# Optimization experiments

Hardware: AMD Instinct MI355X
Metric: run time of the kernel (lower is better)

Reference implementation:

```python
import jax, jax.numpy as jnp
import numpy as np

N = 8192        # nodes
NFEAT = 256     # input feature dim
NHID = 64       # per-head hidden dim
NHEADS = 4
NCLASS = 121    # PPI label count
ALPHA = 0.2     # LeakyReLU negative slope
NEG_INF = jnp.float32(-9e15)  # pyGAT's mask fill value


def setup_inputs() -> dict:
    key = jax.random.key(0)
    k = jax.random.split(key, 6)
    x = jax.random.normal(k[0], (N, NFEAT), dtype=jnp.float32)
    adj = (jax.random.uniform(k[1], (N, N)) < 0.01).astype(jnp.float32)
    idx = jnp.arange(N)
    adj = adj.at[idx, idx].set(1.0)
    # per-head first-layer params: W [H, nfeat, nhid], a [H, 2*nhid]
    Ws = jax.random.normal(k[2], (NHEADS, NFEAT, NHID), dtype=jnp.float32) * 0.1
    a_heads = jax.random.normal(k[3], (NHEADS, 2 * NHID), dtype=jnp.float32) * 0.1
    # output attention layer params
    W_out = jax.random.normal(k[4], (NHEADS * NHID, NCLASS), dtype=jnp.float32) * 0.1
    a_out = jax.random.normal(k[5], (2 * NCLASS,), dtype=jnp.float32) * 0.1
    return {"x": x, "adj": adj, "Ws": Ws, "a_heads": a_heads,
            "W_out": W_out, "a_out": a_out}


def _gat_head(x, adj, W, a, concat):
    # Dense GraphAttentionLayer (pyGAT), eval mode (dropout off).
    Wh = x @ W                                   # [N, d]
    d = W.shape[1]
    f_src = Wh @ a[:d]                           # [N]  score contribution of node i
    f_dst = Wh @ a[d:]                           # [N]  score contribution of node j
    e = jax.nn.leaky_relu(f_src[:, None] + f_dst[None, :], ALPHA)  # [N, N]
    e = jnp.where(adj > 0, e, NEG_INF)
    att = jax.nn.softmax(e, axis=-1)             # [N, N]
    h = att @ Wh                                 # [N, d]
    return jax.nn.elu(h) if concat else h


def reference(x, adj, Ws, a_heads, W_out, a_out):
    # first multi-head layer (concat=True, elu), vmapped over heads
    heads = jax.vmap(lambda W, a: _gat_head(x, adj, W, a, True))(Ws, a_heads)  # [H, N, nhid]
    h_cat = jnp.transpose(heads, (1, 0, 2)).reshape(x.shape[0], NHEADS * NHID)  # torch.cat(dim=1)
    # output attention layer (concat=False -> raw aggregation)
    return _gat_head(h_cat, adj, W_out, a_out, False)  # [N, nclass]
```

## Files before the change

kernel.cpp:

```cpp
#include <hip/hip_runtime.h>
#include <math.h>

#define N_NODES 8192
#define NFEAT 256
#define NHID 64
#define NHEADS 4
#define NCLASS 121
#define NCPAD 128
#define CAP 256
#define LRALPHA 0.2f

__global__ __launch_bounds__(256) void build_csr(const float* __restrict__ adj,
                                                 int* __restrict__ nbr,
                                                 int* __restrict__ deg) {
    int row = blockIdx.x;
    __shared__ int cnt;
    if (threadIdx.x == 0) cnt = 0;
    __syncthreads();
    const float4* arow = (const float4*)(adj + (size_t)row * N_NODES);
    for (int j4 = threadIdx.x; j4 < N_NODES / 4; j4 += 256) {
        float4 v = arow[j4];
        if (v.x > 0.f) { int s = atomicAdd(&cnt, 1); if (s < CAP) nbr[row * CAP + s] = j4 * 4 + 0; }
        if (v.y > 0.f) { int s = atomicAdd(&cnt, 1); if (s < CAP) nbr[row * CAP + s] = j4 * 4 + 1; }
        if (v.z > 0.f) { int s = atomicAdd(&cnt, 1); if (s < CAP) nbr[row * CAP + s] = j4 * 4 + 2; }
        if (v.w > 0.f) { int s = atomicAdd(&cnt, 1); if (s < CAP) nbr[row * CAP + s] = j4 * 4 + 3; }
    }
    __syncthreads();
    if (threadIdx.x == 0) deg[row] = cnt < CAP ? cnt : CAP;
}

__global__ __launch_bounds__(256) void pad_params(const float* __restrict__ Wout,
                                                  const float* __restrict__ aout,
                                                  float* __restrict__ Wpad,
                                                  float* __restrict__ apad) {
    int idx = blockIdx.x * 256 + threadIdx.x;
    if (idx < 256 * NCPAD) {
        int k = idx >> 7, c = idx & 127;
        Wpad[idx] = (c < NCLASS) ? Wout[k * NCLASS + c] : 0.f;
    }
    if (idx < 256) {
        int c = idx & 127;
        float v = 0.f;
        if (c < NCLASS) v = (idx < 128) ? aout[c] : aout[NCLASS + c];
        apad[idx] = v;
    }
}

__global__ __launch_bounds__(256) void gemm1(const float* __restrict__ x,
                                             const float* __restrict__ Ws,
                                             float* __restrict__ Wh1) {
    int h = blockIdx.y;
    int r0 = blockIdx.x * 64;
    __shared__ float xs[64][260];
    for (int t = threadIdx.x; t < 64 * 64; t += 256) {
        int r = t >> 6, c4 = t & 63;
        *(float4*)&xs[r][c4 * 4] = *(const float4*)(x + (size_t)(r0 + r) * NFEAT + c4 * 4);
    }
    __syncthreads();
    int d = threadIdx.x & 63;
    int rb = (threadIdx.x >> 6) * 16;
    const float* W = Ws + (size_t)h * NFEAT * NHID + d;
    float acc[16] = {};
    for (int k4 = 0; k4 < NFEAT; k4 += 4) {
        float b0 = W[(k4 + 0) * NHID];
        float b1 = W[(k4 + 1) * NHID];
        float b2 = W[(k4 + 2) * NHID];
        float b3 = W[(k4 + 3) * NHID];
#pragma unroll
        for (int r = 0; r < 16; r++) {
            float4 a = *(const float4*)&xs[rb + r][k4];
            acc[r] += a.x * b0 + a.y * b1 + a.z * b2 + a.w * b3;
        }
    }
#pragma unroll
    for (int r = 0; r < 16; r++)
        Wh1[((size_t)(r0 + rb + r) * NHEADS + h) * NHID + d] = acc[r];
}

__global__ __launch_bounds__(256) void attn_coef1(const float* __restrict__ Wh1,
                                                  const float* __restrict__ a_heads,
                                                  float* __restrict__ fs1,
                                                  float* __restrict__ fd1) {
    int i = blockIdx.x;
    int h = threadIdx.x >> 6, lane = threadIdx.x & 63;
    float wh = Wh1[((size_t)i * NHEADS + h) * NHID + lane];
    float s = wh * a_heads[h * 2 * NHID + lane];
    float dd = wh * a_heads[h * 2 * NHID + NHID + lane];
#pragma unroll
    for (int o = 32; o > 0; o >>= 1) { s += __shfl_down(s, o); dd += __shfl_down(dd, o); }
    if (lane == 0) { fs1[h * N_NODES + i] = s; fd1[h * N_NODES + i] = dd; }
}

__global__ __launch_bounds__(256) void attn_agg1(const int* __restrict__ nbr,
                                                 const int* __restrict__ deg,
                                                 const float* __restrict__ Wh1,
                                                 const float* __restrict__ fs1,
                                                 const float* __restrict__ fd1,
                                                 float* __restrict__ hcat) {
    int i = blockIdx.x;
    int h = threadIdx.x >> 6, lane = threadIdx.x & 63;
    __shared__ float ebuf[NHEADS][CAP + 1];
    __shared__ int nbrs[CAP];
    __shared__ float inv_s[NHEADS];
    __shared__ float part[NHEADS][256];
    int dg = deg[i];
    for (int t = threadIdx.x; t < dg; t += 256) nbrs[t] = nbr[i * CAP + t];
    __syncthreads();
    float fsi = fs1[h * N_NODES + i];
    const float* fdh = fd1 + h * N_NODES;
    float m = -3.4e38f;
    for (int t = lane; t < dg; t += 64) {
        float e = fsi + fdh[nbrs[t]];
        e = e > 0.f ? e : LRALPHA * e;
        ebuf[h][t] = e;
        m = fmaxf(m, e);
    }
#pragma unroll
    for (int o = 32; o > 0; o >>= 1) m = fmaxf(m, __shfl_xor(m, o));
    float s = 0.f;
    for (int t = lane; t < dg; t += 64) {
        float p = __expf(ebuf[h][t] - m);
        ebuf[h][t] = p;
        s += p;
    }
#pragma unroll
    for (int o = 32; o > 0; o >>= 1) s += __shfl_xor(s, o);
    if (lane == 0) inv_s[h] = 1.f / s;
    __syncthreads();
    int w = h;
    int hh = lane >> 4;
    float4 acc = make_float4(0.f, 0.f, 0.f, 0.f);
    int t = w;
    for (; t + 8 <= dg; t += 8) {
        int j0 = nbrs[t], j1 = nbrs[t + 4];
        float4 v0 = ((const float4*)(Wh1 + (size_t)j0 * 256))[lane];
        float4 v1 = ((const float4*)(Wh1 + (size_t)j1 * 256))[lane];
        float p0 = ebuf[hh][t], p1 = ebuf[hh][t + 4];
        acc.x += p0 * v0.x; acc.y += p0 * v0.y; acc.z += p0 * v0.z; acc.w += p0 * v0.w;
        acc.x += p1 * v1.x; acc.y += p1 * v1.y; acc.z += p1 * v1.z; acc.w += p1 * v1.w;
    }
    for (; t < dg; t += 4) {
        int j = nbrs[t];
        float4 v = ((const float4*)(Wh1 + (size_t)j * 256))[lane];
        float p = ebuf[hh][t];
        acc.x += p * v.x; acc.y += p * v.y; acc.z += p * v.z; acc.w += p * v.w;
    }
    ((float4*)part[w])[lane] = acc;
    __syncthreads();
    int dim = threadIdx.x;
    float r = part[0][dim] + part[1][dim] + part[2][dim] + part[3][dim];
    r *= inv_s[dim >> 6];
    r = r > 0.f ? r : expm1f(r);
    hcat[(size_t)i * 256 + dim] = r;
}

__global__ __launch_bounds__(256) void gemm2(const float* __restrict__ hcat,
                                             const float* __restrict__ Wpad,
                                             float* __restrict__ Wh2) {
    int r0 = blockIdx.x * 64;
    __shared__ float xs[64][260];
    for (int t = threadIdx.x; t < 64 * 64; t += 256) {
        int r = t >> 6, c4 = t & 63;
        *(float4*)&xs[r][c4 * 4] = *(const float4*)(hcat + (size_t)(r0 + r) * 256 + c4 * 4);
    }
    __syncthreads();
    int c0 = (threadIdx.x & 63) * 2;
    int rb = (threadIdx.x >> 6) * 16;
    float acc0[16] = {}, acc1[16] = {};
    for (int k4 = 0; k4 < 256; k4 += 4) {
        float2 b0 = *(const float2*)&Wpad[(k4 + 0) * NCPAD + c0];
        float2 b1 = *(const float2*)&Wpad[(k4 + 1) * NCPAD + c0];
        float2 b2 = *(const float2*)&Wpad[(k4 + 2) * NCPAD + c0];
        float2 b3 = *(const float2*)&Wpad[(k4 + 3) * NCPAD + c0];
#pragma unroll
        for (int r = 0; r < 16; r++) {
            float4 a = *(const float4*)&xs[rb + r][k4];
            acc0[r] += a.x * b0.x + a.y * b1.x + a.z * b2.x + a.w * b3.x;
            acc1[r] += a.x * b0.y + a.y * b1.y + a.z * b2.y + a.w * b3.y;
        }
    }
#pragma unroll
    for (int r = 0; r < 16; r++) {
        float2 v = make_float2(acc0[r], acc1[r]);
        *(float2*)&Wh2[(size_t)(r0 + rb + r) * NCPAD + c0] = v;
    }
}

__global__ __launch_bounds__(256) void attn_coef2(const float* __restrict__ Wh2,
                                                  const float* __restrict__ apad,
                                                  float* __restrict__ fs2,
                                                  float* __restrict__ fd2) {
    int i = blockIdx.x * 4 + (threadIdx.x >> 6);
    int lane = threadIdx.x & 63;
    float w0 = Wh2[(size_t)i * NCPAD + lane];
    float w1 = Wh2[(size_t)i * NCPAD + 64 + lane];
    float s = w0 * apad[lane] + w1 * apad[64 + lane];
    float dd = w0 * apad[128 + lane] + w1 * apad[192 + lane];
#pragma unroll
    for (int o = 32; o > 0; o >>= 1) { s += __shfl_down(s, o); dd += __shfl_down(dd, o); }
    if (lane == 0) { fs2[i] = s; fd2[i] = dd; }
}

__global__ __launch_bounds__(256) void attn_agg2(const int* __restrict__ nbr,
                                                 const int* __restrict__ deg,
                                                 const float* __restrict__ Wh2,
                                                 const float* __restrict__ fs2,
                                                 const float* __restrict__ fd2,
                                                 float* __restrict__ out) {
    int i = blockIdx.x;
    int w = threadIdx.x >> 6, lane = threadIdx.x & 63;
    __shared__ float ebuf[CAP];
    __shared__ int nbrs[CAP];
    __shared__ float red[4];
    __shared__ float part[4][128];
    __shared__ float inv_s;
    int dg = deg[i];
    for (int t = threadIdx.x; t < dg; t += 256) nbrs[t] = nbr[i * CAP + t];
    __syncthreads();
    float fsi = fs2[i];
    float m = -3.4e38f;
    for (int t = threadIdx.x; t < dg; t += 256) {
        float e = fsi + fd2[nbrs[t]];
        e = e > 0.f ? e : LRALPHA * e;
        ebuf[t] = e;
        m = fmaxf(m, e);
    }
#pragma unroll
    for (int o = 32; o > 0; o >>= 1) m = fmaxf(m, __shfl_xor(m, o));
    if (lane == 0) red[w] = m;
    __syncthreads();
    m = fmaxf(fmaxf(red[0], red[1]), fmaxf(red[2], red[3]));
    float s = 0.f;
    for (int t = threadIdx.x; t < dg; t += 256) {
        float p = __expf(ebuf[t] - m);
        ebuf[t] = p;
        s += p;
    }
#pragma unroll
    for (int o = 32; o > 0; o >>= 1) s += __shfl_xor(s, o);
    __syncthreads();
    if (lane == 0) red[w] = s;
    __syncthreads();
    if (threadIdx.x == 0) inv_s = 1.f / (red[0] + red[1] + red[2] + red[3]);
    __syncthreads();
    float2 acc = make_float2(0.f, 0.f);
    int t = w;
    for (; t + 8 <= dg; t += 8) {
        int j0 = nbrs[t], j1 = nbrs[t + 4];
        float2 v0 = ((const float2*)(Wh2 + (size_t)j0 * NCPAD))[lane];
        float2 v1 = ((const float2*)(Wh2 + (size_t)j1 * NCPAD))[lane];
        float p0 = ebuf[t], p1 = ebuf[t + 4];
        acc.x += p0 * v0.x; acc.y += p0 * v0.y;
        acc.x += p1 * v1.x; acc.y += p1 * v1.y;
    }
    for (; t < dg; t += 4) {
        int j = nbrs[t];
        float2 v = ((const float2*)(Wh2 + (size_t)j * NCPAD))[lane];
        float p = ebuf[t];
        acc.x += p * v.x; acc.y += p * v.y;
    }
    ((float2*)part[w])[lane] = acc;
    __syncthreads();
    if (threadIdx.x < NCPAD) {
        int dim = threadIdx.x;
        float r = (part[0][dim] + part[1][dim] + part[2][dim] + part[3][dim]) * inv_s;
        if (dim < NCLASS) out[(size_t)i * NCLASS + dim] = r;
    }
}


extern "C" void kernel_launch(void* const* d_in, const int* in_sizes, int n_in,
                              void* d_out, int out_size, void* d_ws, size_t ws_size,
                              hipStream_t stream) {
    const float* x       = (const float*)d_in[0];
    const float* adj     = (const float*)d_in[1];
    const float* Ws      = (const float*)d_in[2];
    const float* a_heads = (const float*)d_in[3];
    const float* Wout    = (const float*)d_in[4];
    const float* aout    = (const float*)d_in[5];
    float* out = (float*)d_out;

    char* ws = (char*)d_ws;
    size_t off = 0;
    auto alloc = [&](size_t bytes) { void* p = ws + off; off = (off + bytes + 255) & ~(size_t)255; return p; };
    int*   nbr  = (int*)  alloc((size_t)N_NODES * CAP * 4);
    int*   deg  = (int*)  alloc((size_t)N_NODES * 4);
    float* Wh1  = (float*)alloc((size_t)N_NODES * NHEADS * NHID * 4);
    float* fs1  = (float*)alloc((size_t)NHEADS * N_NODES * 4);
    float* fd1  = (float*)alloc((size_t)NHEADS * N_NODES * 4);
    float* hcat = (float*)alloc((size_t)N_NODES * NHEADS * NHID * 4);
    float* Wh2  = (float*)alloc((size_t)N_NODES * NCPAD * 4);
    float* fs2  = (float*)alloc((size_t)N_NODES * 4);
    float* fd2  = (float*)alloc((size_t)N_NODES * 4);
    float* Wpad = (float*)alloc((size_t)256 * NCPAD * 4);
    float* apad = (float*)alloc((size_t)256 * 4);

    build_csr<<<N_NODES, 256, 0, stream>>>(adj, nbr, deg);
    pad_params<<<128, 256, 0, stream>>>(Wout, aout, Wpad, apad);
    gemm1<<<dim3(N_NODES / 64, NHEADS), 256, 0, stream>>>(x, Ws, Wh1);
    attn_coef1<<<N_NODES, 256, 0, stream>>>(Wh1, a_heads, fs1, fd1);
    attn_agg1<<<N_NODES, 256, 0, stream>>>(nbr, deg, Wh1, fs1, fd1, hcat);
    gemm2<<<N_NODES / 64, 256, 0, stream>>>(hcat, Wpad, Wh2);
    attn_coef2<<<N_NODES / 4, 256, 0, stream>>>(Wh2, apad, fs2, fd2);
    attn_agg2<<<N_NODES, 256, 0, stream>>>(nbr, deg, Wh2, fs2, fd2, out);
}
```

Measured before the change: 532.8 us.

## Fuse CSR build, param padding, layer-1 GEMM and attention coefficients into one launch

Merges build_csr, pad_params and gemm1 into a single heterogeneous kernel that dispatches on block index. The GEMM blocks now compute all four heads at once and reduce the attention source/destination scores in-register. The layer-2 coefficient computation is folded into gemm2's epilogue the same way. This removes four kernel launches and the re-reads of Wh1/Wh2 by the separate coefficient kernels. In exchange, the GEMM blocks carry much higher register pressure (64 accumulators plus 16 weight values per thread), and only 128 GEMM blocks share the grid with the 8192 CSR blocks.

```diff
diff --git a/kernel.cpp b/kernel.cpp
--- a/kernel.cpp
+++ b/kernel.cpp
@@ -10,85 +10,120 @@
 #define CAP 256
 #define LRALPHA 0.2f
 
-__global__ __launch_bounds__(256) void build_csr(const float* __restrict__ adj,
-                                                 int* __restrict__ nbr,
-                                                 int* __restrict__ deg) {
-    int row = blockIdx.x;
-    __shared__ int cnt;
-    if (threadIdx.x == 0) cnt = 0;
-    __syncthreads();
-    const float4* arow = (const float4*)(adj + (size_t)row * N_NODES);
-    for (int j4 = threadIdx.x; j4 < N_NODES / 4; j4 += 256) {
-        float4 v = arow[j4];
-        if (v.x > 0.f) { int s = atomicAdd(&cnt, 1); if (s < CAP) nbr[row * CAP + s] = j4 * 4 + 0; }
-        if (v.y > 0.f) { int s = atomicAdd(&cnt, 1); if (s < CAP) nbr[row * CAP + s] = j4 * 4 + 1; }
-        if (v.z > 0.f) { int s = atomicAdd(&cnt, 1); if (s < CAP) nbr[row * CAP + s] = j4 * 4 + 2; }
-        if (v.w > 0.f) { int s = atomicAdd(&cnt, 1); if (s < CAP) nbr[row * CAP + s] = j4 * 4 + 3; }
-    }
-    __syncthreads();
-    if (threadIdx.x == 0) deg[row] = cnt < CAP ? cnt : CAP;
-}
-
-__global__ __launch_bounds__(256) void pad_params(const float* __restrict__ Wout,
-                                                  const float* __restrict__ aout,
-                                                  float* __restrict__ Wpad,
-                                                  float* __restrict__ apad) {
-    int idx = blockIdx.x * 256 + threadIdx.x;
-    if (idx < 256 * NCPAD) {
-        int k = idx >> 7, c = idx & 127;
-        Wpad[idx] = (c < NCLASS) ? Wout[k * NCLASS + c] : 0.f;
-    }
-    if (idx < 256) {
-        int c = idx & 127;
-        float v = 0.f;
-        if (c < NCLASS) v = (idx < 128) ? aout[c] : aout[NCLASS + c];
-        apad[idx] = v;
-    }
-}
-
-__global__ __launch_bounds__(256) void gemm1(const float* __restrict__ x,
-                                             const float* __restrict__ Ws,
-                                             float* __restrict__ Wh1) {
-    int h = blockIdx.y;
-    int r0 = blockIdx.x * 64;
-    __shared__ float xs[64][260];
-    for (int t = threadIdx.x; t < 64 * 64; t += 256) {
-        int r = t >> 6, c4 = t & 63;
-        *(float4*)&xs[r][c4 * 4] = *(const float4*)(x + (size_t)(r0 + r) * NFEAT + c4 * 4);
-    }
-    __syncthreads();
-    int d = threadIdx.x & 63;
-    int rb = (threadIdx.x >> 6) * 16;
-    const float* W = Ws + (size_t)h * NFEAT * NHID + d;
-    float acc[16] = {};
-    for (int k4 = 0; k4 < NFEAT; k4 += 4) {
-        float b0 = W[(k4 + 0) * NHID];
-        float b1 = W[(k4 + 1) * NHID];
-        float b2 = W[(k4 + 2) * NHID];
-        float b3 = W[(k4 + 3) * NHID];
+#define GEMM_BLOCKS 128
+#define CSR_BASE    GEMM_BLOCKS
+#define PAD_BLOCK   (CSR_BASE + N_NODES)
+
+__global__ __launch_bounds__(256) void fused_A(const float* __restrict__ adj,
+                                               const float* __restrict__ x,
+                                               const float* __restrict__ Ws,
+                                               const float* __restrict__ a_heads,
+                                               const float* __restrict__ Wout,
+                                               const float* __restrict__ aout,
+                                               int* __restrict__ nbr,
+                                               int* __restrict__ deg,
+                                               float* __restrict__ Wh1,
+                                               float* __restrict__ fs1,
+                                               float* __restrict__ fd1,
+                                               float* __restrict__ Wpad,
+                                               float* __restrict__ apad) {
+    __shared__ __align__(16) char smem[64 * 132 * 4];
+    int b = blockIdx.x;
+    int tid = threadIdx.x;
+
+    if (b >= CSR_BASE && b < PAD_BLOCK) {
+        int row = b - CSR_BASE;
+        int* cnt = (int*)smem;
+        if (tid == 0) *cnt = 0;
+        __syncthreads();
+        const float4* arow = (const float4*)(adj + (size_t)row * N_NODES);
+        for (int j4 = tid; j4 < N_NODES / 4; j4 += 256) {
+            float4 v = arow[j4];
+            if (v.x > 0.f) { int s = atomicAdd(cnt, 1); if (s < CAP) nbr[row * CAP + s] = j4 * 4 + 0; }
+            if (v.y > 0.f) { int s = atomicAdd(cnt, 1); if (s < CAP) nbr[row * CAP + s] = j4 * 4 + 1; }
+            if (v.z > 0.f) { int s = atomicAdd(cnt, 1); if (s < CAP) nbr[row * CAP + s] = j4 * 4 + 2; }
+            if (v.w > 0.f) { int s = atomicAdd(cnt, 1); if (s < CAP) nbr[row * CAP + s] = j4 * 4 + 3; }
+        }
+        __syncthreads();
+        if (tid == 0) deg[row] = *cnt < CAP ? *cnt : CAP;
+        return;
+    }
+    if (b == PAD_BLOCK) {
+        for (int idx = tid; idx < 256 * NCPAD; idx += 256) {
+            int k = idx >> 7, c = idx & 127;
+            Wpad[idx] = (c < NCLASS) ? Wout[k * NCLASS + c] : 0.f;
+        }
+        if (tid < 256) {
+            int c = tid & 127;
+            float v = 0.f;
+            if (c < NCLASS) v = (tid < 128) ? aout[c] : aout[NCLASS + c];
+            apad[tid] = v;
+        }
+        return;
+    }
+
+    float (*xs)[132] = (float(*)[132])smem;
+    int r0 = b * 64;
+    int d = tid & 63;
+    int rb = (tid >> 6) * 16;
+    float acc[NHEADS][16];
+#pragma unroll
+    for (int h = 0; h < NHEADS; h++)
+#pragma unroll
+        for (int r = 0; r < 16; r++) acc[h][r] = 0.f;
+
+    const float* Wd = Ws + d;
+    for (int ph = 0; ph < 2; ph++) {
+        for (int t = tid; t < 64 * 32; t += 256) {
+            int r = t >> 5, c4 = t & 31;
+            *(float4*)&xs[r][c4 * 4] =
+                *(const float4*)(x + (size_t)(r0 + r) * NFEAT + ph * 128 + c4 * 4);
+        }
+        __syncthreads();
+        for (int k4 = 0; k4 < 128; k4 += 4) {
+            int kg = ph * 128 + k4;
+            float bb[NHEADS][4];
+#pragma unroll
+            for (int h = 0; h < NHEADS; h++)
+#pragma unroll
+                for (int kk = 0; kk < 4; kk++)
+                    bb[h][kk] = Wd[(size_t)h * NFEAT * NHID + (kg + kk) * NHID];
+#pragma unroll
+            for (int r = 0; r < 16; r++) {
+                float4 a = *(const float4*)&xs[rb + r][k4];
+#pragma unroll
+                for (int h = 0; h < NHEADS; h++)
+                    acc[h][r] += a.x * bb[h][0] + a.y * bb[h][1] +
+                                 a.z * bb[h][2] + a.w * bb[h][3];
+            }
+        }
+        __syncthreads();
+    }
+#pragma unroll
+    for (int h = 0; h < NHEADS; h++)
+#pragma unroll
+        for (int r = 0; r < 16; r++)
+            Wh1[(size_t)(r0 + rb + r) * 256 + h * NHID + d] = acc[h][r];
+    float asrc[NHEADS], adst[NHEADS];
+#pragma unroll
+    for (int h = 0; h < NHEADS; h++) {
+        asrc[h] = a_heads[h * 2 * NHID + d];
+        adst[h] = a_heads[h * 2 * NHID + NHID + d];
+    }
+#pragma unroll
+    for (int h = 0; h < NHEADS; h++) {
 #pragma unroll
         for (int r = 0; r < 16; r++) {
-            float4 a = *(const float4*)&xs[rb + r][k4];
-            acc[r] += a.x * b0 + a.y * b1 + a.z * b2 + a.w * b3;
-        }
-    }
-#pragma unroll
-    for (int r = 0; r < 16; r++)
-        Wh1[((size_t)(r0 + rb + r) * NHEADS + h) * NHID + d] = acc[r];
-}
-
-__global__ __launch_bounds__(256) void attn_coef1(const float* __restrict__ Wh1,
-                                                  const float* __restrict__ a_heads,
-                                                  float* __restrict__ fs1,
-                                                  float* __restrict__ fd1) {
-    int i = blockIdx.x;
-    int h = threadIdx.x >> 6, lane = threadIdx.x & 63;
-    float wh = Wh1[((size_t)i * NHEADS + h) * NHID + lane];
-    float s = wh * a_heads[h * 2 * NHID + lane];
-    float dd = wh * a_heads[h * 2 * NHID + NHID + lane];
-#pragma unroll
-    for (int o = 32; o > 0; o >>= 1) { s += __shfl_down(s, o); dd += __shfl_down(dd, o); }
-    if (lane == 0) { fs1[h * N_NODES + i] = s; fd1[h * N_NODES + i] = dd; }
+            float s = acc[h][r] * asrc[h];
+            float dd = acc[h][r] * adst[h];
+#pragma unroll
+            for (int o = 32; o > 0; o >>= 1) { s += __shfl_xor(s, o); dd += __shfl_xor(dd, o); }
+            if (d == 0) {
+                fs1[h * N_NODES + r0 + rb + r] = s;
+                fd1[h * N_NODES + r0 + rb + r] = dd;
+            }
+        }
+    }
 }
 
 __global__ __launch_bounds__(256) void attn_agg1(const int* __restrict__ nbr,
@@ -156,7 +191,10 @@
 
 __global__ __launch_bounds__(256) void gemm2(const float* __restrict__ hcat,
                                              const float* __restrict__ Wpad,
-                                             float* __restrict__ Wh2) {
+                                             const float* __restrict__ apad,
+                                             float* __restrict__ Wh2,
+                                             float* __restrict__ fs2,
+                                             float* __restrict__ fd2) {
     int r0 = blockIdx.x * 64;
     __shared__ float xs[64][260];
     for (int t = threadIdx.x; t < 64 * 64; t += 256) {
@@ -164,7 +202,8 @@
         *(float4*)&xs[r][c4 * 4] = *(const float4*)(hcat + (size_t)(r0 + r) * 256 + c4 * 4);
     }
     __syncthreads();
-    int c0 = (threadIdx.x & 63) * 2;
+    int lane = threadIdx.x & 63;
+    int c0 = lane * 2;
     int rb = (threadIdx.x >> 6) * 16;
     float acc0[16] = {}, acc1[16] = {};
     for (int k4 = 0; k4 < 256; k4 += 4) {
@@ -180,25 +219,18 @@
         }
     }
 #pragma unroll
+    for (int r = 0; r < 16; r++)
+        *(float2*)&Wh2[(size_t)(r0 + rb + r) * NCPAD + c0] = make_float2(acc0[r], acc1[r]);
+    float as0 = apad[c0], as1 = apad[c0 + 1];
+    float ad0 = apad[128 + c0], ad1 = apad[128 + c0 + 1];
+#pragma unroll
     for (int r = 0; r < 16; r++) {
-        float2 v = make_float2(acc0[r], acc1[r]);
-        *(float2*)&Wh2[(size_t)(r0 + rb + r) * NCPAD + c0] = v;
-    }
-}
-
-__global__ __launch_bounds__(256) void attn_coef2(const float* __restrict__ Wh2,
-                                                  const float* __restrict__ apad,
-                                                  float* __restrict__ fs2,
-                                                  float* __restrict__ fd2) {
-    int i = blockIdx.x * 4 + (threadIdx.x >> 6);
-    int lane = threadIdx.x & 63;
-    float w0 = Wh2[(size_t)i * NCPAD + lane];
-    float w1 = Wh2[(size_t)i * NCPAD + 64 + lane];
-    float s = w0 * apad[lane] + w1 * apad[64 + lane];
-    float dd = w0 * apad[128 + lane] + w1 * apad[192 + lane];
-#pragma unroll
-    for (int o = 32; o > 0; o >>= 1) { s += __shfl_down(s, o); dd += __shfl_down(dd, o); }
-    if (lane == 0) { fs2[i] = s; fd2[i] = dd; }
+        float s = acc0[r] * as0 + acc1[r] * as1;
+        float dd = acc0[r] * ad0 + acc1[r] * ad1;
+#pragma unroll
+        for (int o = 32; o > 0; o >>= 1) { s += __shfl_xor(s, o); dd += __shfl_xor(dd, o); }
+        if (lane == 0) { fs2[r0 + rb + r] = s; fd2[r0 + rb + r] = dd; }
+    }
 }
 
 __global__ __launch_bounds__(256) void attn_agg2(const int* __restrict__ nbr,
@@ -295,12 +327,9 @@
     float* Wpad = (float*)alloc((size_t)256 * NCPAD * 4);
     float* apad = (float*)alloc((size_t)256 * 4);
 
-    build_csr<<<N_NODES, 256, 0, stream>>>(adj, nbr, deg);
-    pad_params<<<128, 256, 0, stream>>>(Wout, aout, Wpad, apad);
-    gemm1<<<dim3(N_NODES / 64, NHEADS), 256, 0, stream>>>(x, Ws, Wh1);
-    attn_coef1<<<N_NODES, 256, 0, stream>>>(Wh1, a_heads, fs1, fd1);
+    fused_A<<<PAD_BLOCK + 1, 256, 0, stream>>>(adj, x, Ws, a_heads, Wout, aout,
+                                               nbr, deg, Wh1, fs1, fd1, Wpad, apad);
     attn_agg1<<<N_NODES, 256, 0, stream>>>(nbr, deg, Wh1, fs1, fd1, hcat);
-    gemm2<<<N_NODES / 64, 256, 0, stream>>>(hcat, Wpad, Wh2);
-    attn_coef2<<<N_NODES / 4, 256, 0, stream>>>(Wh2, apad, fs2, fd2);
+    gemm2<<<N_NODES / 64, 256, 0, stream>>>(hcat, Wpad, apad, Wh2, fs2, fd2);
     attn_agg2<<<N_NODES, 256, 0, stream>>>(nbr, deg, Wh2, fs2, fd2, out);
 }
```

Result: slower. 593.5 us (+11.4%).
